# Optimization experiments

Measured on AMD Instinct MI355X. Metric: run time of the kernel, lower is better.

The kernel has to match this reference:

```python
import jax, jax.numpy as jnp
import numpy as np

BLOCK = 32  # GGUF Q8_0 block size: one fp scale per 32 int8 quants


def setup_inputs() -> dict:
    key = jax.random.key(0)
    k1, k2, k3, k4 = jax.random.split(key, 4)
    O, I = 4096, 4096
    T = 8192  # tokens (batch*seq)
    x = jax.random.normal(k1, (T, I), dtype=jnp.float32)
    w_q = jax.random.randint(k2, (O, I), 0, 256, dtype=jnp.int32)
    scales = jax.random.uniform(k3, (O, I // BLOCK), dtype=jnp.float32) * 0.05 + 1e-3
    bias = jax.random.normal(k4, (O,), dtype=jnp.float32)
    return {"x": x, "w_q": w_q, "scales": scales, "bias": bias}


def _dequantize(w_q, scales, dtype):
    # Q8_0-style dequant: centered int quants * per-block scale.
    O, I = w_q.shape
    q = (w_q.astype(dtype) - 128.0).reshape(O, I // BLOCK, BLOCK)
    w = q * scales.astype(dtype)[:, :, None]  # [O, I/B, B]
    return w.reshape(O, I)


def reference(x, w_q, scales, bias):
    # cast_bias_weight: dequantize weight+bias to input dtype, then linear.
    dtype = x.dtype
    w = _dequantize(w_q, scales, dtype)          # [O, I]
    b = bias.astype(dtype)                       # [O]
    return jnp.einsum('ti,oi->to', x, w) + b     # [T, O]
```

## Files before the change

kernel.cpp:

```cpp
#include <hip/hip_runtime.h>

using bf16x8 = __attribute__((ext_vector_type(8))) __bf16;
using f32x4  = __attribute__((ext_vector_type(4))) float;

#define BM 256
#define BN 256
#define BK 64

__device__ __forceinline__ void async_load16(const void* g, void* l) {
    __builtin_amdgcn_global_load_lds(
        (const __attribute__((address_space(1))) unsigned int*)g,
        (__attribute__((address_space(3))) unsigned int*)l,
        16, 0, 0);
}

__global__ __launch_bounds__(256) void prep_kernel(
    const float* __restrict__ x, const int* __restrict__ wq,
    const float* __restrict__ sc, __bf16* __restrict__ xb,
    __bf16* __restrict__ wb, int xc, int wc, int I) {
    int c = blockIdx.x * 256 + threadIdx.x;
    if (c < xc) {
        const int i = c * 8;
        const float4 a = *(const float4*)(x + i);
        const float4 b = *(const float4*)(x + i + 4);
        bf16x8 v;
        v[0] = (__bf16)a.x; v[1] = (__bf16)a.y; v[2] = (__bf16)a.z; v[3] = (__bf16)a.w;
        v[4] = (__bf16)b.x; v[5] = (__bf16)b.y; v[6] = (__bf16)b.z; v[7] = (__bf16)b.w;
        *(bf16x8*)(xb + i) = v;
    } else {
        c -= xc;
        if (c >= wc) return;
        const int i = c * 8;
        const int row = i / I;
        const int col = i - row * I;
        const float s = sc[row * (I >> 5) + (col >> 5)];
        const int4 a = *(const int4*)(wq + i);
        const int4 b = *(const int4*)(wq + i + 4);
        bf16x8 v;
        v[0] = (__bf16)((float)(a.x - 128) * s);
        v[1] = (__bf16)((float)(a.y - 128) * s);
        v[2] = (__bf16)((float)(a.z - 128) * s);
        v[3] = (__bf16)((float)(a.w - 128) * s);
        v[4] = (__bf16)((float)(b.x - 128) * s);
        v[5] = (__bf16)((float)(b.y - 128) * s);
        v[6] = (__bf16)((float)(b.z - 128) * s);
        v[7] = (__bf16)((float)(b.w - 128) * s);
        *(bf16x8*)(wb + i) = v;
    }
}

#define REGA 0
#define REGB 65536

#define BARRIER()  __builtin_amdgcn_s_barrier()
#define LGKM0()    asm volatile("s_waitcnt lgkmcnt(0)" ::: "memory")
#define VMCNT2()   asm volatile("s_waitcnt vmcnt(2)" ::: "memory")
#define VMCNT0()   asm volatile("s_waitcnt vmcnt(0)" ::: "memory")
#define PRIO1()    __builtin_amdgcn_s_setprio(1)
#define PRIO0()    __builtin_amdgcn_s_setprio(0)

__global__ __launch_bounds__(512, 2) void gemm_8phase(
    const __bf16* __restrict__ A, const __bf16* __restrict__ B,
    const float* __restrict__ bias, float* __restrict__ C,
    int M, int N, int K) {
    __shared__ char lds[131072] __attribute__((aligned(16)));
    char* const ldsb = lds;

    const int tid  = threadIdx.x;
    const int wave = tid >> 6;
    const int lane = tid & 63;
    const int r = lane & 15;
    const int q = lane >> 4;
    const int wm = (wave >> 2) * 128;
    const int wn = (wave & 3) * 64;

    const int nwg = gridDim.x;
    const int q8 = nwg >> 3, r8 = nwg & 7;
    const int xcd = blockIdx.x & 7, seq = blockIdx.x >> 3;
    const int swz = (xcd < r8 ? xcd * (q8 + 1)
                              : r8 * (q8 + 1) + (xcd - r8) * q8) + seq;
    const int nTiles = N / BN;
    const int row0 = (swz / nTiles) * BM;
    const int col0 = (swz % nTiles) * BN;

    const size_t rowB = (size_t)K * sizeof(__bf16);

    const char* srcA[2];
    const char* srcB[2];
#pragma unroll
    for (int it = 0; it < 2; ++it) {
        const int p   = (it * 512 + tid) * 16;
        const int lin = p ^ (((p >> 7) & 7) << 4);
        const int gr  = lin >> 7;
        const int gc  = lin & 127;
        srcA[it] = (const char*)A + (size_t)(row0 + gr) * rowB + gc;
        srcB[it] = (const char*)B + (size_t)(col0 + gr) * rowB + gc;
    }

#define STAGE(mat, buf, ht, kb) do {                                         \
        async_load16(src##mat[0] + (size_t)(ht) * 128 * rowB + (kb),         \
            ldsb + REG##mat + (buf) * 32768 + (ht) * 16384 + wave * 1024);   \
        async_load16(src##mat[1] + (size_t)(ht) * 128 * rowB + (kb),         \
            ldsb + REG##mat + (buf) * 32768 + (ht) * 16384 + 8192 + wave * 1024); \
    } while (0)

    const int sb0 = (q ^ (r & 7)) * 16;
    const int sb1 = ((4 + q) ^ (r & 7)) * 16;
    const int aBase = REGA + (wm + r) * 128;
    const int bBase = REGB + (wn + r) * 128;

    bf16x8 afr[4][2];
    bf16x8 bfr[4][2];
    f32x4  acc[8][4];
    const f32x4 zero = {0.f, 0.f, 0.f, 0.f};
#pragma unroll
    for (int i = 0; i < 8; ++i)
#pragma unroll
        for (int j = 0; j < 4; ++j) acc[i][j] = zero;

#define LDA4(buf, mb) do { _Pragma("unroll")                                 \
        for (int mm = 0; mm < 4; ++mm) {                                     \
            const char* pa = ldsb + (buf) * 32768 + aBase + ((mb) + mm) * 2048; \
            afr[mm][0] = *(const bf16x8*)(pa + sb0);                         \
            afr[mm][1] = *(const bf16x8*)(pa + sb1);                         \
        } } while (0)

#define LDB2(buf, nb) do { _Pragma("unroll")                                 \
        for (int nn = 0; nn < 2; ++nn) {                                     \
            const char* pb = ldsb + (buf) * 32768 + bBase + ((nb) + nn) * 2048; \
            bfr[(nb) + nn][0] = *(const bf16x8*)(pb + sb0);                  \
            bfr[(nb) + nn][1] = *(const bf16x8*)(pb + sb1);                  \
        } } while (0)

#define QUAD(mb, nb) do { _Pragma("unroll")                                  \
        for (int mm = 0; mm < 4; ++mm) { _Pragma("unroll")                   \
        for (int nn = 0; nn < 2; ++nn) { _Pragma("unroll")                   \
        for (int ks = 0; ks < 2; ++ks)                                       \
            acc[(mb) + mm][(nb) + nn] = __builtin_amdgcn_mfma_f32_16x16x32_bf16( \
                afr[mm][ks], bfr[(nb) + nn][ks], acc[(mb) + mm][(nb) + nn], 0, 0, 0); \
        } } } while (0)

    STAGE(A, 0, 0, 0); STAGE(A, 0, 1, 0);
    STAGE(B, 0, 0, 0); STAGE(B, 0, 1, 0);
    STAGE(A, 1, 0, 128);
    VMCNT2();
    BARRIER();

    const int nIter = K >> 7;
    for (int i = 0; i < nIter; ++i) {
        const int k0 = i << 7;
        const size_t kb1 = (size_t)(k0 + 64) * 2;
        int k2 = k0 + 128; if (k2 >= K) k2 -= K;
        int k3 = k0 + 192; if (k3 >= K) k3 -= K;
        const size_t kb2 = (size_t)k2 * 2;
        const size_t kb3 = (size_t)k3 * 2;

        LDA4(0, 0); LDB2(0, 0);
        STAGE(A, 1, 1, kb1);
        BARRIER(); LGKM0();
        PRIO1(); QUAD(0, 0); PRIO0();
        BARRIER();
        LDB2(0, 2);
        STAGE(B, 1, 0, kb1);
        BARRIER(); LGKM0();
        PRIO1(); QUAD(0, 2); PRIO0();
        BARRIER();
        LDA4(0, 4);
        STAGE(B, 1, 1, kb1);
        BARRIER(); LGKM0();
        PRIO1(); QUAD(4, 2); PRIO0();
        BARRIER();
        STAGE(A, 0, 0, kb2);
        BARRIER(); LGKM0();
        PRIO1(); QUAD(4, 0); PRIO0();
        VMCNT2();
        BARRIER();
        LDA4(1, 0); LDB2(1, 0);
        STAGE(A, 0, 1, kb2);
        BARRIER(); LGKM0();
        PRIO1(); QUAD(0, 0); PRIO0();
        BARRIER();
        LDB2(1, 2);
        STAGE(B, 0, 0, kb2);
        BARRIER(); LGKM0();
        PRIO1(); QUAD(0, 2); PRIO0();
        BARRIER();
        LDA4(1, 4);
        STAGE(B, 0, 1, kb2);
        BARRIER(); LGKM0();
        PRIO1(); QUAD(4, 2); PRIO0();
        BARRIER();
        STAGE(A, 1, 0, kb3);
        BARRIER(); LGKM0();
        PRIO1(); QUAD(4, 0); PRIO0();
        VMCNT2();
        BARRIER();
    }

    VMCNT0();

#pragma unroll
    for (int n = 0; n < 4; ++n) {
        const int col = col0 + wn + n * 16 + r;
        const float bv = bias[col];
#pragma unroll
        for (int m = 0; m < 8; ++m) {
            const int row = row0 + wm + m * 16 + q * 4;
#pragma unroll
            for (int e = 0; e < 4; ++e)
                C[(size_t)(row + e) * N + col] = acc[m][n][e] + bv;
        }
    }
}

__global__ void fallback_kernel(
    const float* __restrict__ x, const int* __restrict__ wq,
    const float* __restrict__ sc, const float* __restrict__ bias,
    float* __restrict__ out, int T, int O, int I) {
    int o = blockIdx.x * 16 + threadIdx.x;
    int t = blockIdx.y * 16 + threadIdx.y;
    if (o >= O || t >= T) return;
    const int nb = I >> 5;
    float s = 0.f;
    for (int b = 0; b < nb; ++b) {
        const float scv = sc[o * nb + b];
        float p = 0.f;
        for (int k = 0; k < 32; ++k)
            p += x[(size_t)t * I + b * 32 + k] *
                 (float)(wq[(size_t)o * I + b * 32 + k] - 128);
        s += scv * p;
    }
    out[(size_t)t * O + o] = s + bias[o];
}

extern "C" void kernel_launch(void* const* d_in, const int* in_sizes, int n_in,
                              void* d_out, int out_size, void* d_ws, size_t ws_size,
                              hipStream_t stream) {
    const float* x    = (const float*)d_in[0];
    const int*   wq   = (const int*)d_in[1];
    const float* sc   = (const float*)d_in[2];
    const float* bias = (const float*)d_in[3];
    float* out = (float*)d_out;

    const long long xn = in_sizes[0];
    const long long wn = in_sizes[1];
    const int O = in_sizes[3];
    const int I = (int)(wn / O);
    const int T = (int)(xn / I);

    const size_t xbBytes = (size_t)T * I * sizeof(__bf16);
    const size_t wbBytes = (size_t)O * I * sizeof(__bf16);

    const bool fast = (ws_size >= xbBytes + wbBytes) &&
                      (T % BM == 0) && (O % BN == 0) && (I % 128 == 0) &&
                      (((long long)T * I) % (8 * 256) == 0);

    if (!fast) {
        dim3 blk(16, 16);
        dim3 grd((O + 15) / 16, (T + 15) / 16);
        hipLaunchKernelGGL(fallback_kernel, grd, blk, 0, stream,
                           x, wq, sc, bias, out, T, O, I);
        return;
    }

    __bf16* xb = (__bf16*)d_ws;
    __bf16* wb = (__bf16*)((char*)d_ws + xbBytes);

    {
        const int xc = T * (I / 8);
        const int wc = O * (I / 8);
        const int blocks = (xc + wc + 255) / 256;
        hipLaunchKernelGGL(prep_kernel, dim3(blocks), dim3(256), 0, stream,
                           x, wq, sc, xb, wb, xc, wc, I);
    }
    const int nwg = (T / BM) * (O / BN);
    hipLaunchKernelGGL(gemm_8phase, dim3(nwg), dim3(512), 0, stream,
                       xb, wb, bias, out, T, O, I);
}
```

Baseline: 495.5 us.

## Split prep into separate x/w kernels and batch GEMM stage loads per phase

Replaces the combined prep kernel with two kernels. prep_x converts x with float4 loads, and prep_w dequantizes with a 2D grid so each row needs no integer division. In the GEMM main loop, both halves of each A or B tile are now issued together at the first phase of each half-iteration rather than spread one per phase, and the wait threshold moves from vmcnt(2) to vmcnt(4). This front-loads global-to-LDS traffic to give it more time to overlap with compute, at the cost of burstier memory issue. The fast-path condition is tightened to I divisible by 1024.

```diff
diff --git a/kernel.cpp b/kernel.cpp
--- a/kernel.cpp
+++ b/kernel.cpp
@@ -1,11 +1,11 @@
 #include <hip/hip_runtime.h>
 
 using bf16x8 = __attribute__((ext_vector_type(8))) __bf16;
+using bf16x4 = __attribute__((ext_vector_type(4))) __bf16;
 using f32x4  = __attribute__((ext_vector_type(4))) float;
 
 #define BM 256
 #define BN 256
-#define BK 64
 
 __device__ __forceinline__ void async_load16(const void* g, void* l) {
     __builtin_amdgcn_global_load_lds(
@@ -14,39 +14,30 @@
         16, 0, 0);
 }
 
-__global__ __launch_bounds__(256) void prep_kernel(
-    const float* __restrict__ x, const int* __restrict__ wq,
-    const float* __restrict__ sc, __bf16* __restrict__ xb,
-    __bf16* __restrict__ wb, int xc, int wc, int I) {
-    int c = blockIdx.x * 256 + threadIdx.x;
-    if (c < xc) {
-        const int i = c * 8;
-        const float4 a = *(const float4*)(x + i);
-        const float4 b = *(const float4*)(x + i + 4);
-        bf16x8 v;
-        v[0] = (__bf16)a.x; v[1] = (__bf16)a.y; v[2] = (__bf16)a.z; v[3] = (__bf16)a.w;
-        v[4] = (__bf16)b.x; v[5] = (__bf16)b.y; v[6] = (__bf16)b.z; v[7] = (__bf16)b.w;
-        *(bf16x8*)(xb + i) = v;
-    } else {
-        c -= xc;
-        if (c >= wc) return;
-        const int i = c * 8;
-        const int row = i / I;
-        const int col = i - row * I;
-        const float s = sc[row * (I >> 5) + (col >> 5)];
-        const int4 a = *(const int4*)(wq + i);
-        const int4 b = *(const int4*)(wq + i + 4);
-        bf16x8 v;
-        v[0] = (__bf16)((float)(a.x - 128) * s);
-        v[1] = (__bf16)((float)(a.y - 128) * s);
-        v[2] = (__bf16)((float)(a.z - 128) * s);
-        v[3] = (__bf16)((float)(a.w - 128) * s);
-        v[4] = (__bf16)((float)(b.x - 128) * s);
-        v[5] = (__bf16)((float)(b.y - 128) * s);
-        v[6] = (__bf16)((float)(b.z - 128) * s);
-        v[7] = (__bf16)((float)(b.w - 128) * s);
-        *(bf16x8*)(wb + i) = v;
-    }
+__global__ __launch_bounds__(256) void prep_x(
+    const float* __restrict__ x, __bf16* __restrict__ xb, int n4) {
+    const int c = blockIdx.x * 256 + threadIdx.x;
+    if (c >= n4) return;
+    const float4 a = ((const float4*)x)[c];
+    bf16x4 v;
+    v[0] = (__bf16)a.x; v[1] = (__bf16)a.y; v[2] = (__bf16)a.z; v[3] = (__bf16)a.w;
+    ((bf16x4*)xb)[c] = v;
+}
+
+__global__ __launch_bounds__(256) void prep_w(
+    const int* __restrict__ wq, const float* __restrict__ sc,
+    __bf16* __restrict__ wb, int I) {
+    const int row = blockIdx.y;
+    const int c = blockIdx.x * 256 + threadIdx.x;
+    const size_t base = (size_t)row * I + (size_t)c * 4;
+    const float s = sc[row * (I >> 5) + (c >> 3)];
+    const int4 a = *(const int4*)(wq + base);
+    bf16x4 v;
+    v[0] = (__bf16)((float)(a.x - 128) * s);
+    v[1] = (__bf16)((float)(a.y - 128) * s);
+    v[2] = (__bf16)((float)(a.z - 128) * s);
+    v[3] = (__bf16)((float)(a.w - 128) * s);
+    *(bf16x4*)(wb + base) = v;
 }
 
 #define REGA 0
@@ -54,7 +45,7 @@
 
 #define BARRIER()  __builtin_amdgcn_s_barrier()
 #define LGKM0()    asm volatile("s_waitcnt lgkmcnt(0)" ::: "memory")
-#define VMCNT2()   asm volatile("s_waitcnt vmcnt(2)" ::: "memory")
+#define VMCNT4()   asm volatile("s_waitcnt vmcnt(4)" ::: "memory")
 #define VMCNT0()   asm volatile("s_waitcnt vmcnt(0)" ::: "memory")
 #define PRIO1()    __builtin_amdgcn_s_setprio(1)
 #define PRIO0()    __builtin_amdgcn_s_setprio(0)
@@ -140,10 +131,10 @@
                 afr[mm][ks], bfr[(nb) + nn][ks], acc[(mb) + mm][(nb) + nn], 0, 0, 0); \
         } } } while (0)
 
-    STAGE(A, 0, 0, 0); STAGE(A, 0, 1, 0);
-    STAGE(B, 0, 0, 0); STAGE(B, 0, 1, 0);
-    STAGE(A, 1, 0, 128);
-    VMCNT2();
+    STAGE(A, 0, 0, 0);   STAGE(A, 0, 1, 0);
+    STAGE(B, 0, 0, 0);   STAGE(B, 0, 1, 0);
+    STAGE(A, 1, 0, 128); STAGE(A, 1, 1, 128);
+    VMCNT4();
     BARRIER();
 
     const int nIter = K >> 7;
@@ -156,44 +147,40 @@
         const size_t kb3 = (size_t)k3 * 2;
 
         LDA4(0, 0); LDB2(0, 0);
-        STAGE(A, 1, 1, kb1);
+        STAGE(B, 1, 0, kb1); STAGE(B, 1, 1, kb1);
         BARRIER(); LGKM0();
         PRIO1(); QUAD(0, 0); PRIO0();
         BARRIER();
         LDB2(0, 2);
-        STAGE(B, 1, 0, kb1);
         BARRIER(); LGKM0();
         PRIO1(); QUAD(0, 2); PRIO0();
         BARRIER();
         LDA4(0, 4);
-        STAGE(B, 1, 1, kb1);
         BARRIER(); LGKM0();
         PRIO1(); QUAD(4, 2); PRIO0();
         BARRIER();
-        STAGE(A, 0, 0, kb2);
+        STAGE(A, 0, 0, kb2); STAGE(A, 0, 1, kb2);
         BARRIER(); LGKM0();
         PRIO1(); QUAD(4, 0); PRIO0();
-        VMCNT2();
+        VMCNT4();
         BARRIER();
         LDA4(1, 0); LDB2(1, 0);
-        STAGE(A, 0, 1, kb2);
+        STAGE(B, 0, 0, kb2); STAGE(B, 0, 1, kb2);
         BARRIER(); LGKM0();
         PRIO1(); QUAD(0, 0); PRIO0();
         BARRIER();
         LDB2(1, 2);
-        STAGE(B, 0, 0, kb2);
         BARRIER(); LGKM0();
         PRIO1(); QUAD(0, 2); PRIO0();
         BARRIER();
         LDA4(1, 4);
-        STAGE(B, 0, 1, kb2);
         BARRIER(); LGKM0();
         PRIO1(); QUAD(4, 2); PRIO0();
         BARRIER();
-        STAGE(A, 1, 0, kb3);
+        STAGE(A, 1, 0, kb3); STAGE(A, 1, 1, kb3);
         BARRIER(); LGKM0();
         PRIO1(); QUAD(4, 0); PRIO0();
-        VMCNT2();
+        VMCNT4();
         BARRIER();
     }
 
@@ -252,8 +239,8 @@
     const size_t wbBytes = (size_t)O * I * sizeof(__bf16);
 
     const bool fast = (ws_size >= xbBytes + wbBytes) &&
-                      (T % BM == 0) && (O % BN == 0) && (I % 128 == 0) &&
-                      (((long long)T * I) % (8 * 256) == 0);
+                      (T % BM == 0) && (O % BN == 0) && (I % 1024 == 0) &&
+                      (((long long)T * I) % 1024 == 0);
 
     if (!fast) {
         dim3 blk(16, 16);
@@ -267,11 +254,11 @@
     __bf16* wb = (__bf16*)((char*)d_ws + xbBytes);
 
     {
-        const int xc = T * (I / 8);
-        const int wc = O * (I / 8);
-        const int blocks = (xc + wc + 255) / 256;
-        hipLaunchKernelGGL(prep_kernel, dim3(blocks), dim3(256), 0, stream,
-                           x, wq, sc, xb, wb, xc, wc, I);
+        const int n4 = (int)((long long)T * I / 4);
+        hipLaunchKernelGGL(prep_x, dim3((n4 + 255) / 256), dim3(256), 0, stream,
+                           x, xb, n4);
+        hipLaunchKernelGGL(prep_w, dim3(I / 1024, O), dim3(256), 0, stream,
+                           wq, sc, wb, I);
     }
     const int nwg = (T / BM) * (O / BN);
     hipLaunchKernelGGL(gemm_8phase, dim3(nwg), dim3(512), 0, stream,
```

After: 511.6 us. +3.2%, slower.

## Switch GEMM to 32x32x16 MFMA tiles with reordered staging schedule

Applied to the files above, without the earlier changes.

Replaces the 16x16x32 bf16 MFMA fragments with 32x32x16 MFMA, so each wave now holds 4x2 accumulators of 16 floats instead of 8x4 of 4. LDS fragment loads, the swizzle offsets and the epilogue row/column mapping are rewritten to match. The prefetch order is also changed to preload B for the next stage, and the vmcnt wait is relaxed to 4 outstanding loads. The larger MFMA needs fewer LDS reads per flop and fewer instructions, but it changes register pressure and the overlap between loads and compute.

```diff
diff --git a/kernel.cpp b/kernel.cpp
--- a/kernel.cpp
+++ b/kernel.cpp
@@ -2,10 +2,10 @@
 
 using bf16x8 = __attribute__((ext_vector_type(8))) __bf16;
 using f32x4  = __attribute__((ext_vector_type(4))) float;
+using f32x16 = __attribute__((ext_vector_type(16))) float;
 
 #define BM 256
 #define BN 256
-#define BK 64
 
 __device__ __forceinline__ void async_load16(const void* g, void* l) {
     __builtin_amdgcn_global_load_lds(
@@ -54,12 +54,12 @@
 
 #define BARRIER()  __builtin_amdgcn_s_barrier()
 #define LGKM0()    asm volatile("s_waitcnt lgkmcnt(0)" ::: "memory")
-#define VMCNT2()   asm volatile("s_waitcnt vmcnt(2)" ::: "memory")
+#define VMCNT4()   asm volatile("s_waitcnt vmcnt(4)" ::: "memory")
 #define VMCNT0()   asm volatile("s_waitcnt vmcnt(0)" ::: "memory")
 #define PRIO1()    __builtin_amdgcn_s_setprio(1)
 #define PRIO0()    __builtin_amdgcn_s_setprio(0)
 
-__global__ __launch_bounds__(512, 2) void gemm_8phase(
+__global__ __launch_bounds__(512, 2) void gemm_8ph32(
     const __bf16* __restrict__ A, const __bf16* __restrict__ B,
     const float* __restrict__ bias, float* __restrict__ C,
     int M, int N, int K) {
@@ -69,8 +69,8 @@
     const int tid  = threadIdx.x;
     const int wave = tid >> 6;
     const int lane = tid & 63;
-    const int r = lane & 15;
-    const int q = lane >> 4;
+    const int l31  = lane & 31;
+    const int h    = lane >> 5;
     const int wm = (wave >> 2) * 128;
     const int wn = (wave & 3) * 64;
 
@@ -104,46 +104,47 @@
             ldsb + REG##mat + (buf) * 32768 + (ht) * 16384 + 8192 + wave * 1024); \
     } while (0)
 
-    const int sb0 = (q ^ (r & 7)) * 16;
-    const int sb1 = ((4 + q) ^ (r & 7)) * 16;
-    const int aBase = REGA + (wm + r) * 128;
-    const int bBase = REGB + (wn + r) * 128;
-
-    bf16x8 afr[4][2];
-    bf16x8 bfr[4][2];
-    f32x4  acc[8][4];
-    const f32x4 zero = {0.f, 0.f, 0.f, 0.f};
-#pragma unroll
-    for (int i = 0; i < 8; ++i)
-#pragma unroll
-        for (int j = 0; j < 4; ++j) acc[i][j] = zero;
-
-#define LDA4(buf, mb) do { _Pragma("unroll")                                 \
-        for (int mm = 0; mm < 4; ++mm) {                                     \
-            const char* pa = ldsb + (buf) * 32768 + aBase + ((mb) + mm) * 2048; \
-            afr[mm][0] = *(const bf16x8*)(pa + sb0);                         \
-            afr[mm][1] = *(const bf16x8*)(pa + sb1);                         \
+    int s16[4];
+#pragma unroll
+    for (int ks = 0; ks < 4; ++ks)
+        s16[ks] = ((ks * 2 + h) ^ (lane & 7)) * 16;
+    const int aBase = REGA + (wm >> 7) * 16384 + l31 * 128;
+    const int bBase = REGB + (wn >> 7) * 16384 + ((wn & 127) + l31) * 128;
+
+    bf16x8 afr[2][4];
+    bf16x8 bfr[2][4];
+    f32x16 acc[4][2];
+#pragma unroll
+    for (int i = 0; i < 4; ++i)
+#pragma unroll
+        for (int j = 0; j < 2; ++j)
+#pragma unroll
+            for (int e = 0; e < 16; ++e) acc[i][j][e] = 0.f;
+
+#define LDA2(buf, fp) do { _Pragma("unroll")                                 \
+        for (int fm = 0; fm < 2; ++fm) { _Pragma("unroll")                   \
+            for (int ks = 0; ks < 4; ++ks)                                   \
+                afr[fm][ks] = *(const bf16x8*)(ldsb + (buf) * 32768 + aBase  \
+                                               + ((fp) + fm) * 4096 + s16[ks]); \
         } } while (0)
 
-#define LDB2(buf, nb) do { _Pragma("unroll")                                 \
-        for (int nn = 0; nn < 2; ++nn) {                                     \
-            const char* pb = ldsb + (buf) * 32768 + bBase + ((nb) + nn) * 2048; \
-            bfr[(nb) + nn][0] = *(const bf16x8*)(pb + sb0);                  \
-            bfr[(nb) + nn][1] = *(const bf16x8*)(pb + sb1);                  \
+#define LDB1(buf, g) do { _Pragma("unroll")                                  \
+        for (int ks = 0; ks < 4; ++ks)                                       \
+            bfr[g][ks] = *(const bf16x8*)(ldsb + (buf) * 32768 + bBase       \
+                                          + (g) * 4096 + s16[ks]);           \
+    } while (0)
+
+#define OCT(fp, g) do { _Pragma("unroll")                                    \
+        for (int ks = 0; ks < 4; ++ks) { _Pragma("unroll")                   \
+            for (int fm = 0; fm < 2; ++fm)                                   \
+                acc[(fp) + fm][g] = __builtin_amdgcn_mfma_f32_32x32x16_bf16( \
+                    afr[fm][ks], bfr[g][ks], acc[(fp) + fm][g], 0, 0, 0);    \
         } } while (0)
 
-#define QUAD(mb, nb) do { _Pragma("unroll")                                  \
-        for (int mm = 0; mm < 4; ++mm) { _Pragma("unroll")                   \
-        for (int nn = 0; nn < 2; ++nn) { _Pragma("unroll")                   \
-        for (int ks = 0; ks < 2; ++ks)                                       \
-            acc[(mb) + mm][(nb) + nn] = __builtin_amdgcn_mfma_f32_16x16x32_bf16( \
-                afr[mm][ks], bfr[(nb) + nn][ks], acc[(mb) + mm][(nb) + nn], 0, 0, 0); \
-        } } } while (0)
-
-    STAGE(A, 0, 0, 0); STAGE(A, 0, 1, 0);
-    STAGE(B, 0, 0, 0); STAGE(B, 0, 1, 0);
-    STAGE(A, 1, 0, 128);
-    VMCNT2();
+    STAGE(A, 0, 0, 0);  STAGE(A, 0, 1, 0);
+    STAGE(B, 0, 0, 0);  STAGE(B, 0, 1, 0);
+    STAGE(B, 1, 0, 128); STAGE(B, 1, 1, 128);
+    VMCNT4();
     BARRIER();
 
     const int nIter = K >> 7;
@@ -155,60 +156,62 @@
         const size_t kb2 = (size_t)k2 * 2;
         const size_t kb3 = (size_t)k3 * 2;
 
-        LDA4(0, 0); LDB2(0, 0);
+        LDA2(0, 0); LDB1(0, 0);
+        STAGE(A, 1, 0, kb1);
+        BARRIER(); LGKM0();
+        PRIO1(); OCT(0, 0); PRIO0();
+        BARRIER();
+        LDB1(0, 1);
         STAGE(A, 1, 1, kb1);
         BARRIER(); LGKM0();
-        PRIO1(); QUAD(0, 0); PRIO0();
-        BARRIER();
-        LDB2(0, 2);
-        STAGE(B, 1, 0, kb1);
-        BARRIER(); LGKM0();
-        PRIO1(); QUAD(0, 2); PRIO0();
-        BARRIER();
-        LDA4(0, 4);
-        STAGE(B, 1, 1, kb1);
-        BARRIER(); LGKM0();
-        PRIO1(); QUAD(4, 2); PRIO0();
-        BARRIER();
+        PRIO1(); OCT(0, 1); PRIO0();
+        BARRIER();
+        LDA2(0, 2);
+        STAGE(B, 0, 0, kb2);
+        BARRIER(); LGKM0();
+        PRIO1(); OCT(2, 1); PRIO0();
+        BARRIER();
+        STAGE(B, 0, 1, kb2);
+        BARRIER(); LGKM0();
+        PRIO1(); OCT(2, 0); PRIO0();
+        VMCNT4();
+        BARRIER();
+        LDA2(1, 0); LDB1(1, 0);
         STAGE(A, 0, 0, kb2);
         BARRIER(); LGKM0();
-        PRIO1(); QUAD(4, 0); PRIO0();
-        VMCNT2();
-        BARRIER();
-        LDA4(1, 0); LDB2(1, 0);
+        PRIO1(); OCT(0, 0); PRIO0();
+        BARRIER();
+        LDB1(1, 1);
         STAGE(A, 0, 1, kb2);
         BARRIER(); LGKM0();
-        PRIO1(); QUAD(0, 0); PRIO0();
-        BARRIER();
-        LDB2(1, 2);
-        STAGE(B, 0, 0, kb2);
-        BARRIER(); LGKM0();
-        PRIO1(); QUAD(0, 2); PRIO0();
-        BARRIER();
-        LDA4(1, 4);
-        STAGE(B, 0, 1, kb2);
-        BARRIER(); LGKM0();
-        PRIO1(); QUAD(4, 2); PRIO0();
-        BARRIER();
-        STAGE(A, 1, 0, kb3);
-        BARRIER(); LGKM0();
-        PRIO1(); QUAD(4, 0); PRIO0();
-        VMCNT2();
+        PRIO1(); OCT(0, 1); PRIO0();
+        BARRIER();
+        LDA2(1, 2);
+        STAGE(B, 1, 0, kb3);
+        BARRIER(); LGKM0();
+        PRIO1(); OCT(2, 1); PRIO0();
+        BARRIER();
+        STAGE(B, 1, 1, kb3);
+        BARRIER(); LGKM0();
+        PRIO1(); OCT(2, 0); PRIO0();
+        VMCNT4();
         BARRIER();
     }
 
     VMCNT0();
 
 #pragma unroll
-    for (int n = 0; n < 4; ++n) {
-        const int col = col0 + wn + n * 16 + r;
+    for (int g = 0; g < 2; ++g) {
+        const int col = col0 + wn + g * 32 + l31;
         const float bv = bias[col];
 #pragma unroll
-        for (int m = 0; m < 8; ++m) {
-            const int row = row0 + wm + m * 16 + q * 4;
-#pragma unroll
-            for (int e = 0; e < 4; ++e)
-                C[(size_t)(row + e) * N + col] = acc[m][n][e] + bv;
+        for (int f = 0; f < 4; ++f) {
+            const int rbase = row0 + wm + f * 32 + 4 * h;
+#pragma unroll
+            for (int reg = 0; reg < 16; ++reg) {
+                const int row = rbase + (reg & 3) + 8 * (reg >> 2);
+                C[(size_t)row * N + col] = acc[f][g][reg] + bv;
+            }
         }
     }
 }
@@ -253,7 +256,7 @@
 
     const bool fast = (ws_size >= xbBytes + wbBytes) &&
                       (T % BM == 0) && (O % BN == 0) && (I % 128 == 0) &&
-                      (((long long)T * I) % (8 * 256) == 0);
+                      (((long long)T * I) % 8 == 0);
 
     if (!fast) {
         dim3 blk(16, 16);
@@ -267,13 +270,13 @@
     __bf16* wb = (__bf16*)((char*)d_ws + xbBytes);
 
     {
-        const int xc = T * (I / 8);
-        const int wc = O * (I / 8);
+        const int xc = (int)((long long)T * I / 8);
+        const int wc = (int)((long long)O * I / 8);
         const int blocks = (xc + wc + 255) / 256;
         hipLaunchKernelGGL(prep_kernel, dim3(blocks), dim3(256), 0, stream,
                            x, wq, sc, xb, wb, xc, wc, I);
     }
     const int nwg = (T / BM) * (O / BN);
-    hipLaunchKernelGGL(gemm_8phase, dim3(nwg), dim3(512), 0, stream,
+    hipLaunchKernelGGL(gemm_8ph32, dim3(nwg), dim3(512), 0, stream,
                        xb, wb, bias, out, T, O, I);
 }
```

Measured after the change: 524.0 us. 5.7% more time.
